# Kernel tuning notes

Measured on AMD Instinct MI355X. Metric: run time of the kernel, lower is better.

The kernel has to match this reference:

```python
import jax, jax.numpy as jnp
import numpy as np

N = 8192          # n_nodes
E = 262144        # n_edges (avg degree 32)
F_IN, H1, H2, H3, OUT6 = 512, 256, 128, 64, 6


def setup_inputs() -> dict:
    key = jax.random.key(0)
    ks = jax.random.split(key, 12)
    x = jax.random.normal(ks[0], (N, F_IN), dtype=jnp.float32)
    adj_rows = jax.random.randint(ks[1], (E,), 0, N, dtype=jnp.int32)
    adj_cols = jax.random.randint(ks[2], (E,), 0, N, dtype=jnp.int32)
    adj_vals = jax.random.uniform(ks[3], (E,), dtype=jnp.float32)
    s = 0.05  # small init scale
    W1 = jax.random.normal(ks[4], (F_IN, H1), dtype=jnp.float32) * s
    W2 = jax.random.normal(ks[5], (H1, H2), dtype=jnp.float32) * s
    W3 = jax.random.normal(ks[6], (H1, H2), dtype=jnp.float32) * s
    dense_W = jax.random.normal(ks[7], (H2, H3), dtype=jnp.float32) * s
    dense_b = jax.random.normal(ks[8], (H3,), dtype=jnp.float32) * s
    dense1_W = jax.random.normal(ks[9], (H3, OUT6), dtype=jnp.float32) * s
    dense1_b = jax.random.normal(ks[10], (OUT6,), dtype=jnp.float32) * s
    return {"x": x, "adj_rows": adj_rows, "adj_cols": adj_cols, "adj_vals": adj_vals,
            "W1": W1, "W2": W2, "W3": W3,
            "dense_W": dense_W, "dense_b": dense_b,
            "dense1_W": dense1_W, "dense1_b": dense1_b}


def reference(x, adj_rows, adj_cols, adj_vals, W1, W2, W3,
              dense_W, dense_b, dense1_W, dense1_b):
    n = x.shape[0]

    def spmm(support):  # sparse [N,N] @ dense [N,D] via COO gather/segment-sum
        gathered = adj_vals[:, None] * support[adj_cols]  # [E, D]
        return jax.ops.segment_sum(gathered, adj_rows, num_segments=n)

    # eval mode: dropout = identity
    hidden1 = jax.nn.relu(spmm(x @ W1))          # gc1, act=relu
    mu0 = spmm(hidden1 @ W2)                     # gc2, act=identity
    logvar0 = spmm(hidden1 @ W3)                 # gc3, act=identity
    # LinearNet.forward never applies its activation -> plain affine
    mu = mu0 @ dense_W + dense_b                 # [N, H3]
    logvar = logvar0 @ dense_W + dense_b         # [N, H3]
    z = mu                                       # reparameterize in eval mode
    adj_rec = z @ z.T                            # InnerProductDecoder, act=identity
    out6 = z @ dense1_W + dense1_b               # dense1, [N, 6]
    return (adj_rec, out6, mu, logvar)
```

## Files before the change

kernel.cpp:

```cpp
#include <hip/hip_runtime.h>
#include <hip/hip_bf16.h>

#define N_NODES 8192
#define N_EDGES 262144

typedef __attribute__((ext_vector_type(8))) short short8;
typedef __attribute__((ext_vector_type(4))) float f32x4;

__global__ void k_hist(const int* __restrict__ rows, int* __restrict__ counts) {
    int e = blockIdx.x * 256 + threadIdx.x;
    if (e < N_EDGES) atomicAdd(&counts[rows[e]], 1);
}

__global__ void k_scan(const int* __restrict__ counts, int* __restrict__ offs) {
    __shared__ int part[1024];
    int t = threadIdx.x;
    int base = t * 8;
    int loc[8];
    int s = 0;
#pragma unroll
    for (int i = 0; i < 8; i++) { loc[i] = s; s += counts[base + i]; }
    part[t] = s;
    __syncthreads();
    for (int off = 1; off < 1024; off <<= 1) {
        int v = (t >= off) ? part[t - off] : 0;
        __syncthreads();
        part[t] += v;
        __syncthreads();
    }
    int prev = (t == 0) ? 0 : part[t - 1];
#pragma unroll
    for (int i = 0; i < 8; i++) offs[base + i] = prev + loc[i];
    if (t == 1023) offs[N_NODES] = part[1023];
}

__global__ void k_scatter(const int* __restrict__ rows, const int* __restrict__ colsIn,
                          const float* __restrict__ valsIn, const int* __restrict__ offs,
                          int* __restrict__ cursor, int* __restrict__ colsOut,
                          float* __restrict__ valsOut) {
    int e = blockIdx.x * 256 + threadIdx.x;
    if (e >= N_EDGES) return;
    int r = rows[e];
    int p = atomicAdd(&cursor[r], 1);
    int idx = offs[r] + p;
    colsOut[idx] = colsIn[e];
    valsOut[idx] = valsIn[e];
}

__global__ void k_concat_w23(const float* __restrict__ W2, const float* __restrict__ W3,
                             float* __restrict__ W23) {
    int i = blockIdx.x * 256 + threadIdx.x;
    int k = i >> 8, j = i & 255;
    W23[i] = (j < 128) ? W2[k * 128 + j] : W3[k * 128 + (j - 128)];
}

__global__ __launch_bounds__(256) void k_gemm(const float* __restrict__ A, int lda,
                                              const float* __restrict__ B, int ldb,
                                              float* __restrict__ C, int ldc, int K,
                                              const float* __restrict__ bias) {
    __shared__ float sA[16][68];
    __shared__ float sB[16][68];
    int tx = threadIdx.x, ty = threadIdx.y;
    int t = ty * 16 + tx;
    int row0 = blockIdx.y * 64, col0 = blockIdx.x * 64;
    int am = t >> 2, ak = (t & 3) * 4;
    int bk = t >> 4, bn = (t & 15) * 4;
    float acc[4][4] = {};
    for (int k0 = 0; k0 < K; k0 += 16) {
        float4 av = *(const float4*)&A[(size_t)(row0 + am) * lda + k0 + ak];
        float4 bv = *(const float4*)&B[(size_t)(k0 + bk) * ldb + col0 + bn];
        sA[ak + 0][am] = av.x; sA[ak + 1][am] = av.y;
        sA[ak + 2][am] = av.z; sA[ak + 3][am] = av.w;
        *(float4*)&sB[bk][bn] = bv;
        __syncthreads();
#pragma unroll
        for (int k = 0; k < 16; k++) {
            float4 a4 = *(const float4*)&sA[k][ty * 4];
            float4 b4 = *(const float4*)&sB[k][tx * 4];
            float ar[4] = {a4.x, a4.y, a4.z, a4.w};
            float br[4] = {b4.x, b4.y, b4.z, b4.w};
#pragma unroll
            for (int a = 0; a < 4; a++)
#pragma unroll
                for (int b = 0; b < 4; b++) acc[a][b] += ar[a] * br[b];
        }
        __syncthreads();
    }
#pragma unroll
    for (int a = 0; a < 4; a++) {
        int row = row0 + ty * 4 + a;
        int col = col0 + tx * 4;
        float4 r = make_float4(acc[a][0], acc[a][1], acc[a][2], acc[a][3]);
        if (bias) { r.x += bias[col]; r.y += bias[col + 1]; r.z += bias[col + 2]; r.w += bias[col + 3]; }
        *(float4*)&C[(size_t)row * ldc + col] = r;
    }
}

__global__ __launch_bounds__(256) void k_spmm(const int* __restrict__ offs,
                                              const int* __restrict__ cols,
                                              const float* __restrict__ vals,
                                              const float* __restrict__ in,
                                              float* __restrict__ out, int relu) {
    const int row = blockIdx.x;
    const int d = threadIdx.x;
    int s = offs[row], e = offs[row + 1];
    float acc = 0.f;
    __shared__ int sc[256];
    __shared__ float sv[256];
    for (int base = s; base < e; base += 256) {
        int n = e - base;
        if (n > 256) n = 256;
        int idx = base + threadIdx.x;
        if (threadIdx.x < n) { sc[threadIdx.x] = cols[idx]; sv[threadIdx.x] = vals[idx]; }
        __syncthreads();
        for (int i = 0; i < n; i++) acc += sv[i] * in[(size_t)sc[i] * 256 + d];
        __syncthreads();
    }
    out[(size_t)row * 256 + d] = relu ? fmaxf(acc, 0.f) : acc;
}

__global__ __launch_bounds__(256) void k_out6(const float* __restrict__ Z,
                                              const float* __restrict__ W,
                                              const float* __restrict__ b,
                                              float* __restrict__ out) {
    __shared__ float sW[384];
    int t = threadIdx.x;
    for (int i = t; i < 384; i += 256) sW[i] = W[i];
    __syncthreads();
    int row = blockIdx.x * 256 + t;
    float acc[6];
#pragma unroll
    for (int j = 0; j < 6; j++) acc[j] = b[j];
    for (int k = 0; k < 64; k++) {
        float zv = Z[(size_t)row * 64 + k];
#pragma unroll
        for (int j = 0; j < 6; j++) acc[j] += zv * sW[k * 6 + j];
    }
#pragma unroll
    for (int j = 0; j < 6; j++) out[(size_t)row * 6 + j] = acc[j];
}

__global__ void k_f32_to_bf16(const float* __restrict__ in, __hip_bfloat16* __restrict__ out,
                              int n) {
    int i = blockIdx.x * 256 + threadIdx.x;
    if (i < n) out[i] = __float2bfloat16(in[i]);
}

__global__ __launch_bounds__(256) void k_zzt_mfma(const __hip_bfloat16* __restrict__ Zh,
                                                  float* __restrict__ C) {
    int t = threadIdx.x;
    int lane = t & 63;
    int w = t >> 6;
    int I = blockIdx.y * 128 + (w >> 1) * 64;
    int J = blockIdx.x * 128 + (w & 1) * 64;
    int r = lane & 15;
    int koff = (lane >> 4) * 8;

    short8 a[4][2], b[4][2];
#pragma unroll
    for (int m = 0; m < 4; m++) {
#pragma unroll
        for (int kk = 0; kk < 2; kk++) {
            a[m][kk] = *(const short8*)(Zh + (size_t)(I + m * 16 + r) * 64 + kk * 32 + koff);
            b[m][kk] = *(const short8*)(Zh + (size_t)(J + m * 16 + r) * 64 + kk * 32 + koff);
        }
    }
    f32x4 acc[4][4];
#pragma unroll
    for (int m = 0; m < 4; m++)
#pragma unroll
        for (int n = 0; n < 4; n++) acc[m][n] = (f32x4){0.f, 0.f, 0.f, 0.f};

#pragma unroll
    for (int kk = 0; kk < 2; kk++)
#pragma unroll
        for (int m = 0; m < 4; m++)
#pragma unroll
            for (int n = 0; n < 4; n++)
                acc[m][n] = __builtin_amdgcn_mfma_f32_16x16x32_bf16(a[m][kk], b[n][kk],
                                                                    acc[m][n], 0, 0, 0);

    int crow = (lane >> 4) * 4;
    int ccol = lane & 15;
#pragma unroll
    for (int m = 0; m < 4; m++)
#pragma unroll
        for (int rg = 0; rg < 4; rg++) {
            size_t row = (size_t)(I + m * 16 + crow + rg);
#pragma unroll
            for (int n = 0; n < 4; n++)
                C[row * 8192 + J + n * 16 + ccol] = acc[m][n][rg];
        }
}

extern "C" void kernel_launch(void* const* d_in, const int* in_sizes, int n_in,
                              void* d_out, int out_size, void* d_ws, size_t ws_size,
                              hipStream_t stream) {
    const float* x        = (const float*)d_in[0];
    const int*   adj_rows = (const int*)d_in[1];
    const int*   adj_cols = (const int*)d_in[2];
    const float* adj_vals = (const float*)d_in[3];
    const float* W1       = (const float*)d_in[4];
    const float* W2       = (const float*)d_in[5];
    const float* W3       = (const float*)d_in[6];
    const float* dense_W  = (const float*)d_in[7];
    const float* dense_b  = (const float*)d_in[8];
    const float* dense1_W = (const float*)d_in[9];
    const float* dense1_b = (const float*)d_in[10];

    char* p = (char*)d_ws;
    int* counts = (int*)p;   p += 8192 * 4;
    int* cursor = (int*)p;   p += 8192 * 4;
    int* offs   = (int*)p;   p += 8224 * 4;
    int* scol   = (int*)p;   p += (size_t)N_EDGES * 4;
    float* sval = (float*)p; p += (size_t)N_EDGES * 4;
    float* XW1  = (float*)p; p += (size_t)8192 * 256 * 4;
    float* Hid  = (float*)p; p += (size_t)8192 * 256 * 4;
    float* Tb   = (float*)p; p += (size_t)8192 * 256 * 4;
    float* Mb   = (float*)p; p += (size_t)8192 * 256 * 4;
    float* W23  = (float*)p; p += (size_t)256 * 256 * 4;
    __hip_bfloat16* Zh = (__hip_bfloat16*)p; p += (size_t)8192 * 64 * 2;

    float* out     = (float*)d_out;
    float* adj_rec = out;
    float* out6    = out + (size_t)8192 * 8192;
    float* mu      = out6 + (size_t)8192 * 6;
    float* logvar  = mu + (size_t)8192 * 64;

    dim3 blk(16, 16);

    hipMemsetAsync(counts, 0, 2 * 8192 * 4, stream);
    k_hist<<<N_EDGES / 256, 256, 0, stream>>>(adj_rows, counts);
    k_scan<<<1, 1024, 0, stream>>>(counts, offs);
    k_scatter<<<N_EDGES / 256, 256, 0, stream>>>(adj_rows, adj_cols, adj_vals, offs, cursor,
                                                 scol, sval);
    k_concat_w23<<<256, 256, 0, stream>>>(W2, W3, W23);

    k_gemm<<<dim3(4, 128), blk, 0, stream>>>(x, 512, W1, 256, XW1, 256, 512, nullptr);
    k_spmm<<<8192, 256, 0, stream>>>(offs, scol, sval, XW1, Hid, 1);
    k_gemm<<<dim3(4, 128), blk, 0, stream>>>(Hid, 256, W23, 256, Tb, 256, 256, nullptr);
    k_spmm<<<8192, 256, 0, stream>>>(offs, scol, sval, Tb, Mb, 0);
    k_gemm<<<dim3(1, 128), blk, 0, stream>>>(Mb, 256, dense_W, 64, mu, 64, 128, dense_b);
    k_gemm<<<dim3(1, 128), blk, 0, stream>>>(Mb + 128, 256, dense_W, 64, logvar, 64, 128, dense_b);
    k_out6<<<32, 256, 0, stream>>>(mu, dense1_W, dense1_b, out6);
    k_f32_to_bf16<<<2048, 256, 0, stream>>>(mu, Zh, 8192 * 64);
    k_zzt_mfma<<<dim3(64, 64), dim3(256), 0, stream>>>(Zh, adj_rec);
}
```

Before: 462.9 us.

## Move dense GEMMs to bf16 MFMA and store intermediates in bf16

Converts x, W1 and W2/W3 to bf16 (weights pre-transposed) and replaces the fp32 tiled GEMMs with a bf16 MFMA kernel that writes bf16 outputs. The SpMM gathers now read bf16 rows, which halves gather traffic. The two dense projections are fused into one kernel that reads Mb as [2N,128] and also emits the bf16 Z copy, removing the separate conversion kernel. This trades accuracy of the intermediates and of hidden1 for less memory traffic and faster matrix math, and adds conversion kernels for x and the weights.

```diff
diff --git a/kernel.cpp b/kernel.cpp
--- a/kernel.cpp
+++ b/kernel.cpp
@@ -6,6 +6,15 @@
 
 typedef __attribute__((ext_vector_type(8))) short short8;
 typedef __attribute__((ext_vector_type(4))) float f32x4;
+
+__device__ __forceinline__ unsigned short f2bf(float f) {
+    unsigned int u = __float_as_uint(f);
+    u = (u + 0x7fffu + ((u >> 16) & 1u)) >> 16;
+    return (unsigned short)u;
+}
+__device__ __forceinline__ float bf2f(unsigned short h) {
+    return __uint_as_float((unsigned int)h << 16);
+}
 
 __global__ void k_hist(const int* __restrict__ rows, int* __restrict__ counts) {
     int e = blockIdx.x * 256 + threadIdx.x;
@@ -47,60 +56,101 @@
     valsOut[idx] = valsIn[e];
 }
 
-__global__ void k_concat_w23(const float* __restrict__ W2, const float* __restrict__ W3,
-                             float* __restrict__ W23) {
+__global__ void k_conv_x(const float* __restrict__ in, ushort* __restrict__ out) {
     int i = blockIdx.x * 256 + threadIdx.x;
-    int k = i >> 8, j = i & 255;
-    W23[i] = (j < 128) ? W2[k * 128 + j] : W3[k * 128 + (j - 128)];
-}
-
-__global__ __launch_bounds__(256) void k_gemm(const float* __restrict__ A, int lda,
-                                              const float* __restrict__ B, int ldb,
-                                              float* __restrict__ C, int ldc, int K,
-                                              const float* __restrict__ bias) {
-    __shared__ float sA[16][68];
-    __shared__ float sB[16][68];
-    int tx = threadIdx.x, ty = threadIdx.y;
-    int t = ty * 16 + tx;
-    int row0 = blockIdx.y * 64, col0 = blockIdx.x * 64;
-    int am = t >> 2, ak = (t & 3) * 4;
-    int bk = t >> 4, bn = (t & 15) * 4;
-    float acc[4][4] = {};
-    for (int k0 = 0; k0 < K; k0 += 16) {
-        float4 av = *(const float4*)&A[(size_t)(row0 + am) * lda + k0 + ak];
-        float4 bv = *(const float4*)&B[(size_t)(k0 + bk) * ldb + col0 + bn];
-        sA[ak + 0][am] = av.x; sA[ak + 1][am] = av.y;
-        sA[ak + 2][am] = av.z; sA[ak + 3][am] = av.w;
-        *(float4*)&sB[bk][bn] = bv;
-        __syncthreads();
-#pragma unroll
-        for (int k = 0; k < 16; k++) {
-            float4 a4 = *(const float4*)&sA[k][ty * 4];
-            float4 b4 = *(const float4*)&sB[k][tx * 4];
-            float ar[4] = {a4.x, a4.y, a4.z, a4.w};
-            float br[4] = {b4.x, b4.y, b4.z, b4.w};
-#pragma unroll
-            for (int a = 0; a < 4; a++)
-#pragma unroll
-                for (int b = 0; b < 4; b++) acc[a][b] += ar[a] * br[b];
-        }
-        __syncthreads();
-    }
-#pragma unroll
-    for (int a = 0; a < 4; a++) {
-        int row = row0 + ty * 4 + a;
-        int col = col0 + tx * 4;
-        float4 r = make_float4(acc[a][0], acc[a][1], acc[a][2], acc[a][3]);
-        if (bias) { r.x += bias[col]; r.y += bias[col + 1]; r.z += bias[col + 2]; r.w += bias[col + 3]; }
-        *(float4*)&C[(size_t)row * ldc + col] = r;
-    }
-}
-
-__global__ __launch_bounds__(256) void k_spmm(const int* __restrict__ offs,
-                                              const int* __restrict__ cols,
-                                              const float* __restrict__ vals,
-                                              const float* __restrict__ in,
-                                              float* __restrict__ out, int relu) {
+    float4 v = ((const float4*)in)[i];
+    ushort4 o = make_ushort4(f2bf(v.x), f2bf(v.y), f2bf(v.z), f2bf(v.w));
+    ((ushort4*)out)[i] = o;
+}
+
+__global__ void k_w1t(const float* __restrict__ W, ushort* __restrict__ Wt) {
+    int i = blockIdx.x * 256 + threadIdx.x;
+    int k = i >> 8, n = i & 255;
+    Wt[n * 512 + k] = f2bf(W[i]);
+}
+
+__global__ void k_w23t(const float* __restrict__ W2, const float* __restrict__ W3,
+                       ushort* __restrict__ Wt) {
+    int i = blockIdx.x * 256 + threadIdx.x;
+    int n = i >> 8, k = i & 255;
+    float v = (n < 128) ? W2[k * 128 + n] : W3[k * 128 + (n - 128)];
+    Wt[i] = f2bf(v);
+}
+
+__global__ __launch_bounds__(256) void k_gemm_mfma(const ushort* __restrict__ A,
+                                                   const ushort* __restrict__ Bt,
+                                                   ushort* __restrict__ C,
+                                                   int K, int ldc) {
+    int t = threadIdx.x;
+    int lane = t & 63;
+    int w = t >> 6;
+    int I = blockIdx.y * 128 + (w >> 1) * 64;
+    int J = blockIdx.x * 128 + (w & 1) * 64;
+    int r = lane & 15;
+    int koff = (lane >> 4) * 8;
+    const ushort* Ab = A + (size_t)(I + r) * K + koff;
+    const ushort* Bb = Bt + (size_t)(J + r) * K + koff;
+    size_t rs = (size_t)16 * K;
+
+    short8 a0[4], b0[4], a1[4], b1[4];
+#pragma unroll
+    for (int m = 0; m < 4; m++) {
+        a0[m] = *(const short8*)(Ab + m * rs);
+        b0[m] = *(const short8*)(Bb + m * rs);
+    }
+    f32x4 acc[4][4];
+#pragma unroll
+    for (int m = 0; m < 4; m++)
+#pragma unroll
+        for (int n = 0; n < 4; n++) acc[m][n] = (f32x4){0.f, 0.f, 0.f, 0.f};
+
+    int nk = K >> 5;
+    for (int kt = 0; kt < nk; kt += 2) {
+        int o1 = (kt + 1) << 5;
+#pragma unroll
+        for (int m = 0; m < 4; m++) {
+            a1[m] = *(const short8*)(Ab + m * rs + o1);
+            b1[m] = *(const short8*)(Bb + m * rs + o1);
+        }
+#pragma unroll
+        for (int m = 0; m < 4; m++)
+#pragma unroll
+            for (int n = 0; n < 4; n++)
+                acc[m][n] = __builtin_amdgcn_mfma_f32_16x16x32_bf16(a0[m], b0[n], acc[m][n], 0, 0, 0);
+        if (kt + 2 < nk) {
+            int o2 = (kt + 2) << 5;
+#pragma unroll
+            for (int m = 0; m < 4; m++) {
+                a0[m] = *(const short8*)(Ab + m * rs + o2);
+                b0[m] = *(const short8*)(Bb + m * rs + o2);
+            }
+        }
+#pragma unroll
+        for (int m = 0; m < 4; m++)
+#pragma unroll
+            for (int n = 0; n < 4; n++)
+                acc[m][n] = __builtin_amdgcn_mfma_f32_16x16x32_bf16(a1[m], b1[n], acc[m][n], 0, 0, 0);
+    }
+
+    int crow = (lane >> 4) * 4;
+    int ccol = lane & 15;
+#pragma unroll
+    for (int m = 0; m < 4; m++)
+#pragma unroll
+        for (int rg = 0; rg < 4; rg++) {
+            size_t row = (size_t)(I + m * 16 + crow + rg);
+#pragma unroll
+            for (int n = 0; n < 4; n++)
+                C[row * ldc + J + n * 16 + ccol] = f2bf(acc[m][n][rg]);
+        }
+}
+
+__global__ __launch_bounds__(256) void k_spmm_h(const int* __restrict__ offs,
+                                                const int* __restrict__ cols,
+                                                const float* __restrict__ vals,
+                                                const ushort* __restrict__ in,
+                                                ushort* __restrict__ outh,
+                                                float* __restrict__ outf, int relu) {
     const int row = blockIdx.x;
     const int d = threadIdx.x;
     int s = offs[row], e = offs[row + 1];
@@ -110,13 +160,66 @@
     for (int base = s; base < e; base += 256) {
         int n = e - base;
         if (n > 256) n = 256;
-        int idx = base + threadIdx.x;
-        if (threadIdx.x < n) { sc[threadIdx.x] = cols[idx]; sv[threadIdx.x] = vals[idx]; }
-        __syncthreads();
-        for (int i = 0; i < n; i++) acc += sv[i] * in[(size_t)sc[i] * 256 + d];
-        __syncthreads();
-    }
-    out[(size_t)row * 256 + d] = relu ? fmaxf(acc, 0.f) : acc;
+        if (d < n) { sc[d] = cols[base + d]; sv[d] = vals[base + d]; }
+        __syncthreads();
+        for (int i = 0; i < n; i++)
+            acc += sv[i] * bf2f(in[(size_t)sc[i] * 256 + d]);
+        __syncthreads();
+    }
+    if (relu) acc = fmaxf(acc, 0.f);
+    if (outh) outh[(size_t)row * 256 + d] = f2bf(acc);
+    else outf[(size_t)row * 256 + d] = acc;
+}
+
+__global__ __launch_bounds__(256) void k_dense(const float* __restrict__ A,
+                                               const float* __restrict__ B,
+                                               const float* __restrict__ bias,
+                                               float* __restrict__ mu,
+                                               float* __restrict__ logvar,
+                                               ushort* __restrict__ Zh) {
+    __shared__ float sA[16][68];
+    __shared__ float sB[16][68];
+    int tx = threadIdx.x, ty = threadIdx.y;
+    int t = ty * 16 + tx;
+    int row0 = blockIdx.x * 64;
+    int am = t >> 2, ak = (t & 3) * 4;
+    int bk = t >> 4, bn = (t & 15) * 4;
+    float acc[4][4] = {};
+    for (int k0 = 0; k0 < 128; k0 += 16) {
+        float4 av = *(const float4*)&A[(size_t)(row0 + am) * 128 + k0 + ak];
+        float4 bv = *(const float4*)&B[(size_t)(k0 + bk) * 64 + bn];
+        sA[ak + 0][am] = av.x; sA[ak + 1][am] = av.y;
+        sA[ak + 2][am] = av.z; sA[ak + 3][am] = av.w;
+        *(float4*)&sB[bk][bn] = bv;
+        __syncthreads();
+#pragma unroll
+        for (int k = 0; k < 16; k++) {
+            float4 a4 = *(const float4*)&sA[k][ty * 4];
+            float4 b4 = *(const float4*)&sB[k][tx * 4];
+            float ar[4] = {a4.x, a4.y, a4.z, a4.w};
+            float br[4] = {b4.x, b4.y, b4.z, b4.w};
+#pragma unroll
+            for (int a = 0; a < 4; a++)
+#pragma unroll
+                for (int b = 0; b < 4; b++) acc[a][b] += ar[a] * br[b];
+        }
+        __syncthreads();
+    }
+#pragma unroll
+    for (int a = 0; a < 4; a++) {
+        int vrow = row0 + ty * 4 + a;
+        int col = tx * 4;
+        float4 rv = make_float4(acc[a][0] + bias[col], acc[a][1] + bias[col + 1],
+                                acc[a][2] + bias[col + 2], acc[a][3] + bias[col + 3]);
+        int nr = vrow >> 1;
+        if (vrow & 1) {
+            *(float4*)&logvar[(size_t)nr * 64 + col] = rv;
+        } else {
+            *(float4*)&mu[(size_t)nr * 64 + col] = rv;
+            ushort4 h = make_ushort4(f2bf(rv.x), f2bf(rv.y), f2bf(rv.z), f2bf(rv.w));
+            *(ushort4*)&Zh[(size_t)nr * 64 + col] = h;
+        }
+    }
 }
 
 __global__ __launch_bounds__(256) void k_out6(const float* __restrict__ Z,
@@ -140,13 +243,7 @@
     for (int j = 0; j < 6; j++) out[(size_t)row * 6 + j] = acc[j];
 }
 
-__global__ void k_f32_to_bf16(const float* __restrict__ in, __hip_bfloat16* __restrict__ out,
-                              int n) {
-    int i = blockIdx.x * 256 + threadIdx.x;
-    if (i < n) out[i] = __float2bfloat16(in[i]);
-}
-
-__global__ __launch_bounds__(256) void k_zzt_mfma(const __hip_bfloat16* __restrict__ Zh,
+__global__ __launch_bounds__(256) void k_zzt_mfma(const ushort* __restrict__ Zh,
                                                   float* __restrict__ C) {
     int t = threadIdx.x;
     int lane = t & 63;
@@ -209,17 +306,19 @@
     const float* dense1_b = (const float*)d_in[10];
 
     char* p = (char*)d_ws;
-    int* counts = (int*)p;   p += 8192 * 4;
-    int* cursor = (int*)p;   p += 8192 * 4;
-    int* offs   = (int*)p;   p += 8224 * 4;
-    int* scol   = (int*)p;   p += (size_t)N_EDGES * 4;
-    float* sval = (float*)p; p += (size_t)N_EDGES * 4;
-    float* XW1  = (float*)p; p += (size_t)8192 * 256 * 4;
-    float* Hid  = (float*)p; p += (size_t)8192 * 256 * 4;
-    float* Tb   = (float*)p; p += (size_t)8192 * 256 * 4;
-    float* Mb   = (float*)p; p += (size_t)8192 * 256 * 4;
-    float* W23  = (float*)p; p += (size_t)256 * 256 * 4;
-    __hip_bfloat16* Zh = (__hip_bfloat16*)p; p += (size_t)8192 * 64 * 2;
+    int* counts  = (int*)p;    p += 8192 * 4;
+    int* cursor  = (int*)p;    p += 8192 * 4;
+    int* offs    = (int*)p;    p += 8224 * 4;
+    int* scol    = (int*)p;    p += (size_t)N_EDGES * 4;
+    float* sval  = (float*)p;  p += (size_t)N_EDGES * 4;
+    ushort* xh   = (ushort*)p; p += (size_t)8192 * 512 * 2;
+    ushort* W1t  = (ushort*)p; p += (size_t)256 * 512 * 2;
+    ushort* W23t = (ushort*)p; p += (size_t)256 * 256 * 2;
+    ushort* XW1h = (ushort*)p; p += (size_t)8192 * 256 * 2;
+    ushort* Hidh = (ushort*)p; p += (size_t)8192 * 256 * 2;
+    ushort* Tbh  = (ushort*)p; p += (size_t)8192 * 256 * 2;
+    float* Mb    = (float*)p;  p += (size_t)8192 * 256 * 4;
+    ushort* Zh   = (ushort*)p; p += (size_t)8192 * 64 * 2;
 
     float* out     = (float*)d_out;
     float* adj_rec = out;
@@ -227,22 +326,20 @@
     float* mu      = out6 + (size_t)8192 * 6;
     float* logvar  = mu + (size_t)8192 * 64;
 
-    dim3 blk(16, 16);
-
     hipMemsetAsync(counts, 0, 2 * 8192 * 4, stream);
     k_hist<<<N_EDGES / 256, 256, 0, stream>>>(adj_rows, counts);
     k_scan<<<1, 1024, 0, stream>>>(counts, offs);
     k_scatter<<<N_EDGES / 256, 256, 0, stream>>>(adj_rows, adj_cols, adj_vals, offs, cursor,
                                                  scol, sval);
-    k_concat_w23<<<256, 256, 0, stream>>>(W2, W3, W23);
-
-    k_gemm<<<dim3(4, 128), blk, 0, stream>>>(x, 512, W1, 256, XW1, 256, 512, nullptr);
-    k_spmm<<<8192, 256, 0, stream>>>(offs, scol, sval, XW1, Hid, 1);
-    k_gemm<<<dim3(4, 128), blk, 0, stream>>>(Hid, 256, W23, 256, Tb, 256, 256, nullptr);
-    k_spmm<<<8192, 256, 0, stream>>>(offs, scol, sval, Tb, Mb, 0);
-    k_gemm<<<dim3(1, 128), blk, 0, stream>>>(Mb, 256, dense_W, 64, mu, 64, 128, dense_b);
-    k_gemm<<<dim3(1, 128), blk, 0, stream>>>(Mb + 128, 256, dense_W, 64, logvar, 64, 128, dense_b);
+    k_conv_x<<<4096, 256, 0, stream>>>(x, xh);
+    k_w1t<<<512, 256, 0, stream>>>(W1, W1t);
+    k_w23t<<<256, 256, 0, stream>>>(W2, W3, W23t);
+
+    k_gemm_mfma<<<dim3(2, 64), 256, 0, stream>>>(xh, W1t, XW1h, 512, 256);
+    k_spmm_h<<<8192, 256, 0, stream>>>(offs, scol, sval, XW1h, Hidh, nullptr, 1);
+    k_gemm_mfma<<<dim3(2, 64), 256, 0, stream>>>(Hidh, W23t, Tbh, 256, 256);
+    k_spmm_h<<<8192, 256, 0, stream>>>(offs, scol, sval, Tbh, nullptr, Mb, 0);
+    k_dense<<<256, dim3(16, 16), 0, stream>>>(Mb, dense_W, dense_b, mu, logvar, Zh);
     k_out6<<<32, 256, 0, stream>>>(mu, dense1_W, dense1_b, out6);
-    k_f32_to_bf16<<<2048, 256, 0, stream>>>(mu, Zh, 8192 * 64);
-    k_zzt_mfma<<<dim3(64, 64), dim3(256), 0, stream>>>(Zh, adj_rec);
-}
+    k_zzt_mfma<<<dim3(64, 64), 256, 0, stream>>>(Zh, adj_rec);
+}
```

New measurement: 425.5 us. -8.1%, faster.
